# Kernel optimization log

Hardware: AMD Instinct MI355X
Metric: run time of the kernel (lower is better)

Reference implementation:

```python
import jax, jax.numpy as jnp
import numpy as np


def _dequantize(qweight, scale, zero_point, bits, group_size):
    """Unpack int32-packed weights and apply group-wise dequantization.

    qweight:    [N, K // (32//bits)] int32, value i within an int32 at shift i*bits
    scale/zp:   [N, K // group_size]
    returns W:  [N, K] float32
    """
    vpi = 32 // bits  # values per int32
    mask = (1 << bits) - 1
    N, packed = qweight.shape
    K = packed * vpi
    shifts = (jnp.arange(vpi, dtype=jnp.int32) * bits)  # [vpi]
    # [N, packed, vpi] -> flatten so value i of each int32 lands at consecutive K positions
    q = (qweight[:, :, None] >> shifts[None, None, :]) & mask
    q = q.reshape(N, K // group_size, group_size).astype(jnp.float32)
    w = scale[:, :, None] * (q - zero_point[:, :, None])  # group-wise dequant
    return w.reshape(N, K)


def setup_inputs() -> dict:
    key = jax.random.key(0)
    k1, k2, k3, k4, k5 = jax.random.split(key, 5)
    B, S, K, N = 4, 2048, 4096, 4096
    bits, group_size = 4, 128
    vpi = 32 // bits
    num_groups = K // group_size
    x = jax.random.normal(k1, (B, S, K), dtype=jnp.float32)
    qweight = jax.random.randint(k2, (N, K // vpi), jnp.iinfo(jnp.int32).min,
                                 jnp.iinfo(jnp.int32).max, dtype=jnp.int32)
    scale = jax.random.uniform(k3, (N, num_groups), dtype=jnp.float32,
                               minval=0.001, maxval=0.02)
    zero_point = jax.random.uniform(k4, (N, num_groups), dtype=jnp.float32,
                                    minval=0.0, maxval=float((1 << bits) - 1))
    bias = jax.random.normal(k5, (N,), dtype=jnp.float32)
    return {"x": x, "qweight": qweight, "scale": scale, "zero_point": zero_point,
            "bias": bias, "bits": bits, "group_size": group_size}


def reference(x, qweight, scale, zero_point, bias, bits, group_size):
    # Fused dequant + GEMM: y = x @ W^T + b, W dequantized from packed int4 groups
    w = _dequantize(qweight, scale, zero_point, bits, group_size)  # [N, K]
    y = jnp.einsum('bsk,nk->bsn', x, w)
    return y + bias
```

## Files before the change

### kernel.cpp

```cpp
#include <hip/hip_runtime.h>

#define KD 4096
#define ND 4096
#define GRP 32

typedef unsigned short u16;
typedef float   f32x4  __attribute__((ext_vector_type(4)));
typedef __bf16  bf16x8 __attribute__((ext_vector_type(8)));
typedef unsigned short u16x8 __attribute__((ext_vector_type(8)));
typedef unsigned short u16x4 __attribute__((ext_vector_type(4)));

__device__ __forceinline__ u16 f2bf(float f) {
  unsigned u = __float_as_uint(f);
  return (u16)((u + 0x7fffu + ((u >> 16) & 1u)) >> 16);
}

__device__ __forceinline__ void async16(const void* g, void* l) {
  __builtin_amdgcn_global_load_lds(
      (const __attribute__((address_space(1))) unsigned int*)g,
      (__attribute__((address_space(3))) unsigned int*)l, 16, 0, 0);
}

__global__ __launch_bounds__(256) void prep_kernel(
    const int* __restrict__ qw, const float* __restrict__ scale,
    const float* __restrict__ zp, u16* __restrict__ wout,
    const float4* __restrict__ x, u16x8* __restrict__ xb) {
  const int b = blockIdx.x, tid = threadIdx.x;
  if (b < 8192) {
    int idx = b * 256 + tid;
    int n = idx >> 9;
    int p = idx & 511;
    int g = p >> 4;
    float s = scale[n * GRP + g];
    float bz = -s * zp[n * GRP + g];
    unsigned q = (unsigned)qw[idx];
    u16x8 hv;
#pragma unroll
    for (int i = 0; i < 8; ++i)
      hv[i] = f2bf(fmaf((float)((q >> (4 * i)) & 15u), s, bz));
    *(u16x8*)(wout + (size_t)idx * 8) = hv;
  } else {
    int i = (b - 8192) * 256 + tid;
    float4 v0 = x[(size_t)i * 2], v1 = x[(size_t)i * 2 + 1];
    u16x8 h;
    h[0] = f2bf(v0.x); h[1] = f2bf(v0.y); h[2] = f2bf(v0.z); h[3] = f2bf(v0.w);
    h[4] = f2bf(v1.x); h[5] = f2bf(v1.y); h[6] = f2bf(v1.z); h[7] = f2bf(v1.w);
    xb[i] = h;
  }
}

template <int XF32, int WQ>
__global__ __launch_bounds__(256, 4) void gemm_kernel(
    const u16*   __restrict__ xb,
    const float* __restrict__ xf,
    const u16*   __restrict__ wb,
    const int*   __restrict__ qw,
    const float* __restrict__ scale,
    const float* __restrict__ zp,
    const float* __restrict__ bias,
    float* __restrict__ out) {
  __shared__ u16 As[128 * 32];
  __shared__ u16 Bs[128 * 32];
  const int tid = threadIdx.x;
  const int l = tid & 63, w = tid >> 6;
  const int m0 = blockIdx.y * 128, n0 = blockIdx.x * 128;
  const int wm = (w >> 1) * 64, wn = (w & 1) * 64;
  const int col = l & 15, quad = l >> 4;
  const int swz = (col >> 1) & 3;
  const int cg = (l & 3) ^ ((l >> 3) & 3);
  f32x4 acc[4][4] = {};

  for (int k0 = 0; k0 < KD; k0 += 32) {
    __syncthreads();

    if constexpr (XF32) {
#pragma unroll
      for (int it = 0; it < 4; ++it) {
        int fi = it * 256 + tid;
        int row = fi >> 3, cs = fi & 7;
        float4 v = *(const float4*)(xf + (size_t)(m0 + row) * KD + k0 + cs * 4);
        u16x4 h;
        h[0] = f2bf(v.x); h[1] = f2bf(v.y); h[2] = f2bf(v.z); h[3] = f2bf(v.w);
        int ch = (cs >> 1) ^ ((row >> 1) & 3);
        *(u16x4*)(&As[row * 32 + ch * 8 + (cs & 1) * 4]) = h;
      }
    } else {
#pragma unroll
      for (int c = 0; c < 2; ++c) {
        int br = (w * 2 + c) * 16;
        const u16* g = xb + (size_t)(m0 + br + (l >> 2)) * KD + k0 + cg * 8;
        async16(g, &As[br * 32]);
      }
    }

    if constexpr (WQ) {
#pragma unroll
      for (int it = 0; it < 2; ++it) {
        int qi = it * 256 + tid;
        int row = qi >> 2, p4 = qi & 3;
        int nrow = n0 + row;
        int g = k0 >> 7;
        float s = scale[nrow * GRP + g];
        float bz = -s * zp[nrow * GRP + g];
        unsigned q = (unsigned)qw[(size_t)nrow * (KD / 8) + (k0 >> 3) + p4];
        u16x8 hv;
#pragma unroll
        for (int i = 0; i < 8; ++i)
          hv[i] = f2bf(fmaf((float)((q >> (4 * i)) & 15u), s, bz));
        *(u16x8*)(&Bs[row * 32 + ((p4 ^ ((row >> 1) & 3)) * 8)]) = hv;
      }
    } else {
#pragma unroll
      for (int c = 0; c < 2; ++c) {
        int br = (w * 2 + c) * 16;
        const u16* g = wb + (size_t)(n0 + br + (l >> 2)) * KD + k0 + cg * 8;
        async16(g, &Bs[br * 32]);
      }
    }

    __syncthreads();

    bf16x8 a[4], b[4];
#pragma unroll
    for (int i = 0; i < 4; ++i)
      a[i] = *(const bf16x8*)&As[(wm + i * 16 + col) * 32 + (quad ^ swz) * 8];
#pragma unroll
    for (int j = 0; j < 4; ++j)
      b[j] = *(const bf16x8*)&Bs[(wn + j * 16 + col) * 32 + (quad ^ swz) * 8];
#pragma unroll
    for (int i = 0; i < 4; ++i)
#pragma unroll
      for (int j = 0; j < 4; ++j)
        acc[i][j] = __builtin_amdgcn_mfma_f32_16x16x32_bf16(a[i], b[j], acc[i][j], 0, 0, 0);
  }

#pragma unroll
  for (int j = 0; j < 4; ++j) {
    int n = n0 + wn + j * 16 + col;
    float bj = bias[n];
#pragma unroll
    for (int i = 0; i < 4; ++i) {
      int mrow = m0 + wm + i * 16 + quad * 4;
#pragma unroll
      for (int r = 0; r < 4; ++r)
        out[(size_t)(mrow + r) * ND + n] = acc[i][j][r] + bj;
    }
  }
}

extern "C" void kernel_launch(void* const* d_in, const int* in_sizes, int n_in,
                              void* d_out, int out_size, void* d_ws, size_t ws_size,
                              hipStream_t stream) {
  const float* x     = (const float*)d_in[0];
  const int*   qw    = (const int*)d_in[1];
  const float* scale = (const float*)d_in[2];
  const float* zp    = (const float*)d_in[3];
  const float* bias  = (const float*)d_in[4];
  float* out = (float*)d_out;

  const int M = in_sizes[0] / KD;
  dim3 grid(ND / 128, M / 128), block(256);

  const size_t needW = (size_t)ND * KD * sizeof(u16);
  const size_t needX = (size_t)M * KD * sizeof(u16);

  if (ws_size >= needW + needX) {
    u16* wb = (u16*)d_ws;
    u16* xb = wb + (size_t)ND * KD;
    int conv_blocks = (M * (KD / 8)) / 256;
    prep_kernel<<<8192 + conv_blocks, 256, 0, stream>>>(
        qw, scale, zp, wb, (const float4*)x, (u16x8*)xb);
    gemm_kernel<0, 0><<<grid, block, 0, stream>>>(xb, x, wb, qw, scale, zp, bias, out);
  } else if (ws_size >= needW) {
    u16* wb = (u16*)d_ws;
    prep_kernel<<<8192, 256, 0, stream>>>(qw, scale, zp, wb, nullptr, nullptr);
    gemm_kernel<1, 0><<<grid, block, 0, stream>>>(nullptr, x, wb, qw, scale, zp, bias, out);
  } else {
    gemm_kernel<1, 1><<<grid, block, 0, stream>>>(nullptr, x, nullptr, qw, scale, zp, bias, out);
  }
}
```

Before: 538.6 us.

## Double the GEMM K-tile to 64 with an 8-way XOR swizzle

The GEMM's K step grows from 32 to 64, which halves the number of barrier pairs and loop iterations and issues twice as many MFMAs per shared-memory fill. LDS tiles double to 16 KB each, and the swizzle becomes an 8-slot XOR on row&7 for both the async global-to-LDS loads and the fragment reads. Launch bounds drop to 3 blocks per CU to allow for the larger footprint. The x conversion prep now has each thread handle one float4 instead of two, which doubles the number of prep blocks.

```diff
diff --git a/kernel.cpp b/kernel.cpp
--- a/kernel.cpp
+++ b/kernel.cpp
@@ -24,7 +24,7 @@
 __global__ __launch_bounds__(256) void prep_kernel(
     const int* __restrict__ qw, const float* __restrict__ scale,
     const float* __restrict__ zp, u16* __restrict__ wout,
-    const float4* __restrict__ x, u16x8* __restrict__ xb) {
+    const float4* __restrict__ x, u16x4* __restrict__ xb) {
   const int b = blockIdx.x, tid = threadIdx.x;
   if (b < 8192) {
     int idx = b * 256 + tid;
@@ -40,17 +40,16 @@
       hv[i] = f2bf(fmaf((float)((q >> (4 * i)) & 15u), s, bz));
     *(u16x8*)(wout + (size_t)idx * 8) = hv;
   } else {
-    int i = (b - 8192) * 256 + tid;
-    float4 v0 = x[(size_t)i * 2], v1 = x[(size_t)i * 2 + 1];
-    u16x8 h;
-    h[0] = f2bf(v0.x); h[1] = f2bf(v0.y); h[2] = f2bf(v0.z); h[3] = f2bf(v0.w);
-    h[4] = f2bf(v1.x); h[5] = f2bf(v1.y); h[6] = f2bf(v1.z); h[7] = f2bf(v1.w);
+    size_t i = (size_t)(b - 8192) * 256 + tid;
+    float4 v = x[i];
+    u16x4 h;
+    h[0] = f2bf(v.x); h[1] = f2bf(v.y); h[2] = f2bf(v.z); h[3] = f2bf(v.w);
     xb[i] = h;
   }
 }
 
 template <int XF32, int WQ>
-__global__ __launch_bounds__(256, 4) void gemm_kernel(
+__global__ __launch_bounds__(256, 3) void gemm_kernel(
     const u16*   __restrict__ xb,
     const float* __restrict__ xf,
     const u16*   __restrict__ wb,
@@ -59,79 +58,84 @@
     const float* __restrict__ zp,
     const float* __restrict__ bias,
     float* __restrict__ out) {
-  __shared__ u16 As[128 * 32];
-  __shared__ u16 Bs[128 * 32];
+  __shared__ u16 As[128 * 64];
+  __shared__ u16 Bs[128 * 64];
   const int tid = threadIdx.x;
   const int l = tid & 63, w = tid >> 6;
   const int m0 = blockIdx.y * 128, n0 = blockIdx.x * 128;
   const int wm = (w >> 1) * 64, wn = (w & 1) * 64;
   const int col = l & 15, quad = l >> 4;
-  const int swz = (col >> 1) & 3;
-  const int cg = (l & 3) ^ ((l >> 3) & 3);
+  const int rsw = col & 7;
+  const int lr = l >> 3;
+  const int csrc = (l & 7) ^ lr;
   f32x4 acc[4][4] = {};
 
-  for (int k0 = 0; k0 < KD; k0 += 32) {
+  for (int k0 = 0; k0 < KD; k0 += 64) {
     __syncthreads();
 
     if constexpr (XF32) {
 #pragma unroll
-      for (int it = 0; it < 4; ++it) {
+      for (int it = 0; it < 8; ++it) {
         int fi = it * 256 + tid;
-        int row = fi >> 3, cs = fi & 7;
+        int row = fi >> 4, cs = fi & 15;
         float4 v = *(const float4*)(xf + (size_t)(m0 + row) * KD + k0 + cs * 4);
         u16x4 h;
         h[0] = f2bf(v.x); h[1] = f2bf(v.y); h[2] = f2bf(v.z); h[3] = f2bf(v.w);
-        int ch = (cs >> 1) ^ ((row >> 1) & 3);
-        *(u16x4*)(&As[row * 32 + ch * 8 + (cs & 1) * 4]) = h;
+        int slot = (cs >> 1) ^ (row & 7);
+        *(u16x4*)(&As[row * 64 + slot * 8 + (cs & 1) * 4]) = h;
       }
     } else {
 #pragma unroll
-      for (int c = 0; c < 2; ++c) {
-        int br = (w * 2 + c) * 16;
-        const u16* g = xb + (size_t)(m0 + br + (l >> 2)) * KD + k0 + cg * 8;
-        async16(g, &As[br * 32]);
+      for (int c = 0; c < 4; ++c) {
+        int br = w * 32 + c * 8;
+        const u16* g = xb + (size_t)(m0 + br + lr) * KD + k0 + csrc * 8;
+        async16(g, &As[br * 64]);
       }
     }
 
     if constexpr (WQ) {
 #pragma unroll
-      for (int it = 0; it < 2; ++it) {
+      for (int it = 0; it < 4; ++it) {
         int qi = it * 256 + tid;
-        int row = qi >> 2, p4 = qi & 3;
+        int row = qi >> 3, p8 = qi & 7;
         int nrow = n0 + row;
         int g = k0 >> 7;
         float s = scale[nrow * GRP + g];
         float bz = -s * zp[nrow * GRP + g];
-        unsigned q = (unsigned)qw[(size_t)nrow * (KD / 8) + (k0 >> 3) + p4];
+        unsigned q = (unsigned)qw[(size_t)nrow * (KD / 8) + (k0 >> 3) + p8];
         u16x8 hv;
 #pragma unroll
         for (int i = 0; i < 8; ++i)
           hv[i] = f2bf(fmaf((float)((q >> (4 * i)) & 15u), s, bz));
-        *(u16x8*)(&Bs[row * 32 + ((p4 ^ ((row >> 1) & 3)) * 8)]) = hv;
+        *(u16x8*)(&Bs[row * 64 + ((p8 ^ (row & 7)) * 8)]) = hv;
       }
     } else {
 #pragma unroll
-      for (int c = 0; c < 2; ++c) {
-        int br = (w * 2 + c) * 16;
-        const u16* g = wb + (size_t)(n0 + br + (l >> 2)) * KD + k0 + cg * 8;
-        async16(g, &Bs[br * 32]);
+      for (int c = 0; c < 4; ++c) {
+        int br = w * 32 + c * 8;
+        const u16* g = wb + (size_t)(n0 + br + lr) * KD + k0 + csrc * 8;
+        async16(g, &Bs[br * 64]);
       }
     }
 
     __syncthreads();
 
-    bf16x8 a[4], b[4];
 #pragma unroll
-    for (int i = 0; i < 4; ++i)
-      a[i] = *(const bf16x8*)&As[(wm + i * 16 + col) * 32 + (quad ^ swz) * 8];
+    for (int kk = 0; kk < 2; ++kk) {
+      bf16x8 a[4], b[4];
+      const int slot = ((kk * 4 + quad) ^ rsw) * 8;
 #pragma unroll
-    for (int j = 0; j < 4; ++j)
-      b[j] = *(const bf16x8*)&Bs[(wn + j * 16 + col) * 32 + (quad ^ swz) * 8];
-#pragma unroll
-    for (int i = 0; i < 4; ++i)
+      for (int i = 0; i < 4; ++i)
+        a[i] = *(const bf16x8*)&As[(wm + i * 16 + col) * 64 + slot];
 #pragma unroll
       for (int j = 0; j < 4; ++j)
-        acc[i][j] = __builtin_amdgcn_mfma_f32_16x16x32_bf16(a[i], b[j], acc[i][j], 0, 0, 0);
+        b[j] = *(const bf16x8*)&Bs[(wn + j * 16 + col) * 64 + slot];
+#pragma unroll
+      for (int i = 0; i < 4; ++i)
+#pragma unroll
+        for (int j = 0; j < 4; ++j)
+          acc[i][j] = __builtin_amdgcn_mfma_f32_16x16x32_bf16(a[i], b[j], acc[i][j], 0, 0, 0);
+    }
   }
 
 #pragma unroll
@@ -167,9 +171,9 @@
   if (ws_size >= needW + needX) {
     u16* wb = (u16*)d_ws;
     u16* xb = wb + (size_t)ND * KD;
-    int conv_blocks = (M * (KD / 8)) / 256;
+    int conv_blocks = (M * (KD / 4)) / 256;
     prep_kernel<<<8192 + conv_blocks, 256, 0, stream>>>(
-        qw, scale, zp, wb, (const float4*)x, (u16x8*)xb);
+        qw, scale, zp, wb, (const float4*)x, (u16x4*)xb);
     gemm_kernel<0, 0><<<grid, block, 0, stream>>>(xb, x, wb, qw, scale, zp, bias, out);
   } else if (ws_size >= needW) {
     u16* wb = (u16*)d_ws;
```

After: 476.1 us. 1.13x faster.
